# Kernel optimization log

Hardware: AMD Instinct MI355X
Metric: run time of the kernel (lower is better)

Reference implementation:

```python
import jax, jax.numpy as jnp
import numpy as np

N, D, A, K, E = 8192, 256, 1024, 65, 4096

def setup_inputs() -> dict:
    key = jax.random.key(0)
    ks = jax.random.split(key, 8)
    s = 0.02  # linear-init scale to keep activations sane
    return {
        "embedding": jax.random.normal(ks[0], (N, D), jnp.float32),
        "data": jax.random.randint(ks[1], (E, 2), 0, N, jnp.int64),
        "Wq": jax.random.normal(ks[2], (D, A), jnp.float32) * s,
        "bq": jnp.zeros((A,), jnp.float32),
        "Wk": jax.random.normal(ks[3], (D, A), jnp.float32) * s,
        "bk": jnp.zeros((A,), jnp.float32),
        "Wv": jax.random.normal(ks[4], (D, A), jnp.float32) * s,
        "bv": jnp.zeros((A,), jnp.float32),
        "W_edge": jax.random.normal(ks[5], (K, A, A), jnp.float32) * s,
    }

def reference(embedding, data, Wq, bq, Wk, bk, Wv, bv, W_edge):
    # NodeSelfAttention: dense full attention over all N nodes
    Q = embedding @ Wq + bq            # [N, A]
    Km = embedding @ Wk + bk           # [N, A]
    V = embedding @ Wv + bv            # [N, A]
    scale = 1.0 / jnp.sqrt(jnp.float32(D))  # note: sqrt(num_feats)=sqrt(256), as in source
    scores = (Q @ Km.T) * scale        # [N, N]
    attn = jax.nn.softmax(scores, axis=-1)
    attn_emb = attn @ V                # [N, A]
    # gather edge endpoints
    h_u = attn_emb[data[:, 0]]         # [E, A]
    h_v = attn_emb[data[:, 1]]         # [E, A]
    # KWayPred: out[e,k] = h_u[e] @ W_edge[k] @ h_v[e]
    # (source computes full ExE matmul per k and takes diag; this is the
    #  equivalent O(E*K*A^2) bilinear-diag form)
    t = jnp.einsum('ed,kdf->ekf', h_u, W_edge)   # [E, K, A]
    out = jnp.einsum('ekf,ef->ek', t, h_v)       # [E, K]
    return out
```

## Files before the change

### kernel.cpp

```cpp
#include <hip/hip_runtime.h>
#include <cstdio>
#include <cstdint>

#define NTOK 8192
#define DIM  256
#define AA   1024
#define KE   65
#define EE   4096

typedef unsigned short u16;
typedef __attribute__((ext_vector_type(4))) float   f32x4;
typedef __attribute__((ext_vector_type(8))) short   bf16x8;
typedef __attribute__((ext_vector_type(8))) unsigned short u16x8;

#define DEVI __device__ __forceinline__

DEVI u16 f2bf(float f) {
  union { float f; unsigned u; } x; x.f = f;
  unsigned r = x.u + 0x7FFFu + ((x.u >> 16) & 1u);
  return (u16)(r >> 16);
}
DEVI float bf2f(u16 h) {
  union { unsigned u; float f; } x; x.u = ((unsigned)h) << 16;
  return x.f;
}

DEVI void gload16(const void* g, void* l) {
  __builtin_amdgcn_global_load_lds(
      (const __attribute__((address_space(1))) void*)g,
      (__attribute__((address_space(3))) void*)l,
      16, 0, 0);
}

DEVI void barx() {
  asm volatile("" ::: "memory");
  __builtin_amdgcn_s_barrier();
  asm volatile("" ::: "memory");
}

DEVI void stage_half(const u16* __restrict__ g0, int ld, char* dst, int tid) {
#pragma unroll
  for (int rr = 0; rr < 2; ++rr) {
    int o = rr * 8192 + (tid >> 6) * 1024 + (tid & 63) * 16;
    int q = o ^ (((o >> 7) & 7) << 4);
    gload16(g0 + (size_t)(q >> 7) * ld + ((q & 127) >> 1),
            dst + rr * 8192 + (tid >> 6) * 1024);
  }
}

template<int EPI, int QMODE>
__global__ __launch_bounds__(512, 2)
void gemm8(const u16* __restrict__ A, int lda,
           const u16* __restrict__ B, int ldb,
           int MT, int NT, int K,
           u16* __restrict__ o_s, float scale, int ldc,
           const u16* __restrict__ Hu, float* __restrict__ o_e,
           int* __restrict__ qcnt)
{
  __shared__ __align__(16) char lds[131072];
  __shared__ int s_next[3];
  char* ldsA = lds;
  char* ldsB = lds + 65536;

  const int tid = threadIdx.x, lane = tid & 63, wave = tid >> 6;
  const int wm = (wave >> 2) * 128;
  const int wn = (wave & 3) * 64;
  const int wnl = (wave & 1) * 64;
  const int KT = K >> 6, KT2 = KT >> 1;
  const int r15 = lane & 15, g16 = (lane >> 4) << 4;

  int xcc;
  asm volatile("s_getreg_b32 %0, hwreg(20, 0, 32)" : "=s"(xcc));
  xcc &= 7;
  const int MPX = MT >> 3;
  const int NQ = NT >> 3, NR = NT & 7;

  const char* Ab_e = ldsA +         (wm >> 7) * 16384;
  const char* Ab_o = ldsA + 32768 + (wm >> 7) * 16384;
  const char* Bb_e = ldsB +         (wn >> 7) * 16384;
  const char* Bb_o = ldsB + 32768 + (wn >> 7) * 16384;

  int dxr = 0;
  auto pop_next = [&]() {
    while (dxr < 8) {
      const int qi = (xcc + dxr) & 7;
      int per, ntb = 0, ntc = 0;
      if constexpr (QMODE == 0) {
        per = (MT * NT) >> 3;
      } else {
        ntc = NQ + (qi < NR ? 1 : 0);
        ntb = qi * NQ + (qi < NR ? qi : NR);
        per = ntc * MT;
      }
      const int idx = atomicAdd(&qcnt[qi], 1);
      if (idx < per) {
        int mt, nt;
        if constexpr (QMODE == 0) {
          mt = qi * MPX + (idx % MPX); nt = idx / MPX;
        } else {
          const int srw = ntc << 3;
          const int sr = idx / srw, rem = idx - sr * srw;
          nt = ntb + (rem >> 3); mt = (sr << 3) + (rem & 7);
        }
        s_next[0] = mt * 256; s_next[1] = nt * 256; s_next[2] = 1;
        return;
      }
      ++dxr;
    }
    s_next[2] = 0;
  };

  if (tid == 0) pop_next();
  __syncthreads();
  int m0 = s_next[0], n0 = s_next[1];
  if (!s_next[2]) return;

#define STAGE_A2(tk, h) do { const int _tk = (tk); \
    if (_tk < KT) stage_half(A + (size_t)(m0 + (h)*128) * lda + (size_t)_tk*64, lda, \
                             ldsA + (_tk & 1) * 32768 + (h) * 16384, tid); \
    else if (have_n) stage_half(A + (size_t)(m0n + (h)*128) * lda + (size_t)(_tk-KT)*64, lda, \
                                ldsA + (_tk & 1) * 32768 + (h) * 16384, tid); } while (0)
#define STAGE_B2(tk, h) do { const int _tk = (tk); \
    if (_tk < KT) stage_half(B + (size_t)(n0 + (h)*128) * ldb + (size_t)_tk*64, ldb, \
                             ldsB + (_tk & 1) * 32768 + (h) * 16384, tid); \
    else if (have_n) stage_half(B + (size_t)(n0n + (h)*128) * ldb + (size_t)(_tk-KT)*64, ldb, \
                                ldsB + (_tk & 1) * 32768 + (h) * 16384, tid); } while (0)
#define RD_A4(base, q) \
  _Pragma("unroll") for (int m = (q)*4; m < (q)*4+4; ++m) \
  _Pragma("unroll") for (int kk = 0; kk < 2; ++kk) { \
    int p = (m*16 + r15)*128 + kk*64 + g16; p ^= ((p>>7)&7)<<4; \
    a[m][kk] = *(const bf16x8*)((base) + p); }
#define RD_B2(base, q) \
  _Pragma("unroll") for (int n = (q)*2; n < (q)*2+2; ++n) \
  _Pragma("unroll") for (int kk = 0; kk < 2; ++kk) { \
    int p = (wnl + n*16 + r15)*128 + kk*64 + g16; p ^= ((p>>7)&7)<<4; \
    b[n][kk] = *(const bf16x8*)((base) + p); }
#define MM(QM, QN) do { \
  __builtin_amdgcn_s_setprio(1); \
  _Pragma("unroll") for (int kk = 0; kk < 2; ++kk) \
  _Pragma("unroll") for (int m = 0; m < 4; ++m) \
  _Pragma("unroll") for (int n = 0; n < 2; ++n) \
    acc[(QM)*4+m][(QN)*2+n] = __builtin_amdgcn_mfma_f32_16x16x32_bf16( \
        a[(QM)*4+m][kk], b[(QN)*2+n][kk], acc[(QM)*4+m][(QN)*2+n], 0, 0, 0); \
  __builtin_amdgcn_s_setprio(0); } while (0)
#define WAIT_LGKM0 do { asm volatile("s_waitcnt lgkmcnt(0)" ::: "memory"); \
                        __builtin_amdgcn_sched_barrier(0); } while (0)
#define KTILE(t, AB, BB) do { \
     \
    RD_B2(BB, 0); RD_A4(AB, 0); \
    STAGE_B2((t) + 1, 1); \
    asm volatile("s_waitcnt lgkmcnt(8)" ::: "memory"); \
    barx(); WAIT_LGKM0; \
    MM(0, 0); \
    barx(); \
     \
    RD_B2(BB, 1); \
    barx(); WAIT_LGKM0; \
    MM(0, 1); \
    barx(); \
     \
    RD_A4(AB, 1); \
    STAGE_B2((t) + 2, 0); \
    barx(); WAIT_LGKM0; \
    MM(1, 1); \
    barx(); \
     \
    STAGE_A2((t) + 2, 0); \
    STAGE_A2((t) + 2, 1); \
    barx(); \
    __builtin_amdgcn_sched_barrier(0); \
    MM(1, 0); \
    if (vm6) asm volatile("s_waitcnt vmcnt(6)" ::: "memory"); \
    else     asm volatile("s_waitcnt vmcnt(0)" ::: "memory"); \
    barx(); } while (0)

  {
    const int m0n = 0, n0n = 0; const bool have_n = false; (void)m0n; (void)n0n; (void)have_n;
    STAGE_A2(0, 0); STAGE_A2(0, 1); STAGE_B2(0, 0); STAGE_B2(0, 1);
    STAGE_B2(1, 0); STAGE_A2(1, 0); STAGE_A2(1, 1);
  }
  asm volatile("s_waitcnt vmcnt(6)" ::: "memory");
  barx();

  while (true) {
    f32x4 acc[8][4];
#pragma unroll
    for (int m = 0; m < 8; ++m)
#pragma unroll
      for (int n = 0; n < 4; ++n) acc[m][n] = f32x4{0.f, 0.f, 0.f, 0.f};

    int m0n = 0, n0n = 0;
    bool have_n = false;

    for (int i = 0; i < KT2; ++i) {
      const int ta = 2 * i, tb = 2 * i + 1;
      if (i == KT2 - 2 && tid == 0) pop_next();
      if (i == KT2 - 1) { m0n = s_next[0]; n0n = s_next[1]; have_n = (s_next[2] != 0); }
      const bool tail = (i == KT2 - 1);
      const bool vm6 = !tail || have_n;
      bf16x8 a[8][2], b[4][2];
      KTILE(ta, Ab_e, Bb_e);
      KTILE(tb, Ab_o, Bb_o);
    }

    const int rgrp = lane >> 4, cid = lane & 15;
    if constexpr (EPI == 1) {
#pragma unroll
      for (int m = 0; m < 8; ++m)
#pragma unroll
        for (int n = 0; n < 4; ++n)
#pragma unroll
          for (int j = 0; j < 4; ++j) {
            int row = m0 + wm + m * 16 + rgrp * 4 + j;
            int col = n0 + wn + n * 16 + cid;
            o_s[(size_t)row * ldc + col] = f2bf(acc[m][n][j] * scale);
          }
    } else {
      const int kidx  = n0 >> 10;
      const int dbase = (n0 & 1023) + wn;
#pragma unroll
      for (int m = 0; m < 8; ++m)
#pragma unroll
        for (int j = 0; j < 4; ++j) {
          int row = m0 + wm + m * 16 + rgrp * 4 + j;
          float p = 0.f;
#pragma unroll
          for (int n = 0; n < 4; ++n)
            p += acc[m][n][j] * bf2f(Hu[(size_t)row * AA + dbase + n * 16 + cid]);
          p += __shfl_xor(p, 1, 64);
          p += __shfl_xor(p, 2, 64);
          p += __shfl_xor(p, 4, 64);
          p += __shfl_xor(p, 8, 64);
          if (cid == 0) atomicAdd(&o_e[(size_t)row * KE + kidx], p);
        }
    }

    if (!have_n) break;
    m0 = m0n; n0 = n0n;
  }
#undef STAGE_A2
#undef STAGE_B2
#undef RD_A4
#undef RD_B2
#undef MM
#undef WAIT_LGKM0
#undef KTILE
}

#define BM 128
#define BN 128
#define BK 64

template<int EPI, bool BF32>
__global__ __launch_bounds__(256)
void gemm_bt(const u16* __restrict__ A, int lda,
             const void* __restrict__ Bptr, int ldb,
             int MT, int NT, int K,
             u16* __restrict__ o_q, u16* __restrict__ o_k, u16* __restrict__ o_vt,
             const float* __restrict__ biasc,
             u16* __restrict__ o_s, float scale, int ldc,
             const u16* __restrict__ Hu, float* __restrict__ o_e)
{
  const int nb  = MT * NT;
  const int per = nb >> 3;
  int bid = blockIdx.x;
  bid = (bid & 7) * per + (bid >> 3);
  const int mt = bid % MT, nt = bid / MT;
  const int m0 = mt * BM, n0 = nt * BN;

  __shared__ u16 As[BM * BK];
  __shared__ u16 Bs[BN * BK];

  const int tid  = threadIdx.x;
  const int lane = tid & 63, wave = tid >> 6;
  const int wm = (wave >> 1) * 64, wn = (wave & 1) * 64;

  f32x4 acc[4][4];
#pragma unroll
  for (int m = 0; m < 4; ++m)
#pragma unroll
    for (int n = 0; n < 4; ++n) acc[m][n] = f32x4{0.f, 0.f, 0.f, 0.f};

  const u16*   Bh = (const u16*)Bptr;
  const float* Bf = (const float*)Bptr;

  const int KT = K / BK;
  for (int kt = 0; kt < KT; ++kt) {
    const int k0 = kt * BK;
#pragma unroll
    for (int it = 0; it < 4; ++it) {
      int o = it * 4096 + wave * 1024 + lane * 16;
      int r = o >> 7;
      int c = (o & 127) >> 1;
      gload16(A + (size_t)(m0 + r) * lda + k0 + c,
              &As[(it * 4096 + wave * 1024) >> 1]);
    }
    if constexpr (!BF32) {
#pragma unroll
      for (int it = 0; it < 4; ++it) {
        int o = it * 4096 + wave * 1024 + lane * 16;
        int r = o >> 7;
        int c = (o & 127) >> 1;
        gload16(Bh + (size_t)(n0 + r) * ldb + k0 + c,
                &Bs[(it * 4096 + wave * 1024) >> 1]);
      }
    } else {
#pragma unroll
      for (int it = 0; it < 8; ++it) {
        int e = it * 1024 + tid * 4;
        int r = e >> 6, c = e & 63;
        const float4 v = *(const float4*)(Bf + (size_t)(n0 + r) * ldb + k0 + c);
        ushort4 h;
        h.x = f2bf(v.x); h.y = f2bf(v.y); h.z = f2bf(v.z); h.w = f2bf(v.w);
        *(ushort4*)&Bs[r * BK + c] = h;
      }
    }
    asm volatile("s_waitcnt vmcnt(0)" ::: "memory");
    __syncthreads();

#pragma unroll
    for (int kk = 0; kk < 2; ++kk) {
      const int ro = lane & 15;
      const int ko = kk * 32 + (lane >> 4) * 8;
      bf16x8 af[4], bfg[4];
#pragma unroll
      for (int m = 0; m < 4; ++m)
        af[m] = *(const bf16x8*)&As[(wm + m * 16 + ro) * BK + ko];
#pragma unroll
      for (int n = 0; n < 4; ++n)
        bfg[n] = *(const bf16x8*)&Bs[(wn + n * 16 + ro) * BK + ko];
#pragma unroll
      for (int m = 0; m < 4; ++m)
#pragma unroll
        for (int n = 0; n < 4; ++n)
          acc[m][n] = __builtin_amdgcn_mfma_f32_16x16x32_bf16(
              af[m], bfg[n], acc[m][n], 0, 0, 0);
    }
    __syncthreads();
  }

  const int rgrp = lane >> 4, cid = lane & 15;

  if constexpr (EPI == 0) {
#pragma unroll
    for (int m = 0; m < 4; ++m)
#pragma unroll
      for (int n = 0; n < 4; ++n)
#pragma unroll
        for (int j = 0; j < 4; ++j) {
          int row = m0 + wm + m * 16 + rgrp * 4 + j;
          int col = n0 + wn + n * 16 + cid;
          float v = acc[m][n][j] + biasc[col];
          u16 h = f2bf(v);
          if (col < 1024)       o_q[(size_t)row * AA + col] = h;
          else if (col < 2048)  o_k[(size_t)row * AA + (col - 1024)] = h;
          else                  o_vt[(size_t)(col - 2048) * NTOK + row] = h;
        }
  } else if constexpr (EPI == 1) {
#pragma unroll
    for (int m = 0; m < 4; ++m)
#pragma unroll
      for (int n = 0; n < 4; ++n)
#pragma unroll
        for (int j = 0; j < 4; ++j) {
          int row = m0 + wm + m * 16 + rgrp * 4 + j;
          int col = n0 + wn + n * 16 + cid;
          o_s[(size_t)row * ldc + col] = f2bf(acc[m][n][j] * scale);
        }
  } else {
    const int kidx  = n0 >> 10;
    const int dbase = (n0 & 1023) + wn;
#pragma unroll
    for (int m = 0; m < 4; ++m)
#pragma unroll
      for (int j = 0; j < 4; ++j) {
        int row = m0 + wm + m * 16 + rgrp * 4 + j;
        float p = 0.f;
#pragma unroll
        for (int n = 0; n < 4; ++n) {
          int d = dbase + n * 16 + cid;
          p += acc[m][n][j] * bf2f(Hu[(size_t)row * AA + d]);
        }
        p += __shfl_xor(p, 1, 64);
        p += __shfl_xor(p, 2, 64);
        p += __shfl_xor(p, 4, 64);
        p += __shfl_xor(p, 8, 64);
        if (cid == 0) atomicAdd(&o_e[(size_t)row * KE + kidx], p);
      }
  }
}

__global__ __launch_bounds__(256)
void softmax_rows(u16* __restrict__ S)
{
  const size_t base = (size_t)blockIdx.x * 8192;
  const int tid = threadIdx.x;
  const int lane = tid & 63, wave = tid >> 6;
  float v[32];
#pragma unroll
  for (int c = 0; c < 4; ++c) {
    u16x8 u = *(const u16x8*)&S[base + c * 2048 + tid * 8];
#pragma unroll
    for (int j = 0; j < 8; ++j) v[c * 8 + j] = bf2f(u[j]);
  }
  float mx = -1e30f;
#pragma unroll
  for (int i = 0; i < 32; ++i) mx = fmaxf(mx, v[i]);
#pragma unroll
  for (int off = 1; off < 64; off <<= 1) mx = fmaxf(mx, __shfl_xor(mx, off, 64));
  __shared__ float r1[4], r2[4];
  if (lane == 0) r1[wave] = mx;
  __syncthreads();
  mx = fmaxf(fmaxf(r1[0], r1[1]), fmaxf(r1[2], r1[3]));

  float s = 0.f;
#pragma unroll
  for (int i = 0; i < 32; ++i) { v[i] = __expf(v[i] - mx); s += v[i]; }
#pragma unroll
  for (int off = 1; off < 64; off <<= 1) s += __shfl_xor(s, off, 64);
  if (lane == 0) r2[wave] = s;
  __syncthreads();
  s = r2[0] + r2[1] + r2[2] + r2[3];
  const float inv = 1.f / s;
#pragma unroll
  for (int c = 0; c < 4; ++c) {
    u16x8 u;
#pragma unroll
    for (int j = 0; j < 8; ++j) u[j] = f2bf(v[c * 8 + j] * inv);
    *(u16x8*)&S[base + c * 2048 + tid * 8] = u;
  }
}

__global__ __launch_bounds__(256)
void gather_rows(const unsigned* __restrict__ dw, const u16* __restrict__ AE,
                 u16* __restrict__ Hu, u16* __restrict__ Hv)
{
  bool i64 = true;
#pragma unroll
  for (int w = 1; w < 32; w += 2) i64 = i64 && (dw[w] == 0u);
  const int e = blockIdx.x;
  const unsigned iu = i64 ? dw[4 * e]     : dw[2 * e];
  const unsigned iv = i64 ? dw[4 * e + 2] : dw[2 * e + 1];
  const int t = threadIdx.x;
  *(ushort4*)&Hu[(size_t)e * AA + t * 4] = *(const ushort4*)&AE[(size_t)iu * AA + t * 4];
  *(ushort4*)&Hv[(size_t)e * AA + t * 4] = *(const ushort4*)&AE[(size_t)iv * AA + t * 4];
}

__global__ __launch_bounds__(256)
void init_misc(float* __restrict__ out_e, const float* __restrict__ bq,
               const float* __restrict__ bk, const float* __restrict__ bv,
               float* __restrict__ biasc, int* __restrict__ qall)
{
  const int i = blockIdx.x * 256 + threadIdx.x;
  if (i < EE * KE) out_e[i] = 0.f;
  if (i < 1024) {
    biasc[i]        = bq[i];
    biasc[1024 + i] = bk[i];
    biasc[2048 + i] = bv[i];
  }
  if (i < 64) qall[i] = 0;
}

__global__ __launch_bounds__(256)
void cvt_f32_bf16_v4(const float* __restrict__ src, u16* __restrict__ dst, int n4)
{
  for (int i = blockIdx.x * 256 + threadIdx.x; i < n4; i += gridDim.x * 256) {
    float4 v = ((const float4*)src)[i];
    ushort4 h; h.x = f2bf(v.x); h.y = f2bf(v.y); h.z = f2bf(v.z); h.w = f2bf(v.w);
    ((ushort4*)dst)[i] = h;
  }
}

__global__ __launch_bounds__(256)
void build_wT(const float* __restrict__ Wq, const float* __restrict__ Wk,
              const float* __restrict__ Wv, u16* __restrict__ WT)
{
  const int nn = blockIdx.x;
  const int d  = threadIdx.x;
  const float* W = (nn < 1024) ? Wq : ((nn < 2048) ? Wk : Wv);
  WT[nn * DIM + d] = f2bf(W[(size_t)d * AA + (nn & 1023)]);
}

extern "C" void kernel_launch(void* const* d_in, const int* in_sizes, int n_in,
                              void* d_out, int out_size, void* d_ws, size_t ws_size,
                              hipStream_t stream)
{
  (void)in_sizes; (void)out_size;
  if (n_in < 9) return;
  const float*    emb  = (const float*)d_in[0];
  const unsigned* data = (const unsigned*)d_in[1];
  const float* Wq = (const float*)d_in[2];
  const float* bq = (const float*)d_in[3];
  const float* Wk = (const float*)d_in[4];
  const float* bk = (const float*)d_in[5];
  const float* Wv = (const float*)d_in[6];
  const float* bv = (const float*)d_in[7];
  const float* We = (const float*)d_in[8];
  float* out = (float*)d_out;

  char* ws = (char*)d_ws;
  size_t off = 0;
  auto alloc = [&](size_t bytes) -> void* {
    void* p = ws + off;
    off += (bytes + 255) & ~(size_t)255;
    return p;
  };
  u16*   emb_b = (u16*)alloc((size_t)NTOK * DIM * 2);
  u16*   WT    = (u16*)alloc((size_t)3072 * DIM * 2);
  float* biasc = (float*)alloc(3072 * 4);
  int*   qall  = (int*)alloc(64 * 4);
  u16*   Qb    = (u16*)alloc((size_t)NTOK * AA * 2);
  u16*   Kb    = (u16*)alloc((size_t)NTOK * AA * 2);
  u16*   Vt    = (u16*)alloc((size_t)AA * NTOK * 2);
  u16*   AE    = (u16*)alloc((size_t)NTOK * AA * 2);
  u16*   Hu    = (u16*)alloc((size_t)EE * AA * 2);
  u16*   Hv    = (u16*)alloc((size_t)EE * AA * 2);

  const size_t webf_bytes = ((size_t)KE * AA * AA * 2 + 255) & ~(size_t)255;
  u16* We_b = nullptr;
  if (off + webf_bytes + (size_t)1024 * NTOK * 2 <= ws_size) {
    We_b = (u16*)(ws + off);
    off += webf_bytes;
  }

  int chunk = 4096;
  while (chunk > 128 && off + (size_t)chunk * NTOK * 2 > ws_size) chunk >>= 1;
  u16* Sc = (u16*)alloc((size_t)chunk * NTOK * 2);
  if (off > ws_size) {
    fprintf(stderr, "kernel_launch: ws too small (need %zu, have %zu)\n", off, ws_size);
    return;
  }

  init_misc<<<(EE * KE) / 256, 256, 0, stream>>>(out, bq, bk, bv, biasc, qall);
  cvt_f32_bf16_v4<<<2048, 256, 0, stream>>>(emb, emb_b, NTOK * DIM / 4);
  build_wT<<<3072, 256, 0, stream>>>(Wq, Wk, Wv, WT);
  if (We_b)
    cvt_f32_bf16_v4<<<4096, 256, 0, stream>>>(We, We_b, KE * AA * AA / 4);

  gemm_bt<0, false><<<64 * 24, 256, 0, stream>>>(
      emb_b, DIM, WT, DIM, 64, 24, DIM,
      Qb, Kb, Vt, biasc, nullptr, 0.f, 0, nullptr, nullptr);

  const int nch = NTOK / chunk;
  for (int ci = 0; ci < nch; ++ci) {
    const u16* Qc = Qb + (size_t)ci * chunk * AA;
    const bool big = ((chunk & 2047) == 0);
    if (big)
      gemm8<1, 1><<<256, 512, 0, stream>>>(
          Qc, AA, Kb, AA, chunk / 256, 32, AA,
          Sc, 0.0625f, NTOK, nullptr, nullptr, qall + 8 * ci);
    else
      gemm_bt<1, false><<<(chunk / 128) * 64, 256, 0, stream>>>(
          Qc, AA, Kb, AA, chunk / 128, 64, AA,
          nullptr, nullptr, nullptr, nullptr, Sc, 0.0625f, NTOK, nullptr, nullptr);
    softmax_rows<<<chunk, 256, 0, stream>>>(Sc);
    gemm_bt<1, false><<<(chunk / 128) * 8, 256, 0, stream>>>(
        Sc, NTOK, Vt, NTOK, chunk / 128, 8, NTOK,
        nullptr, nullptr, nullptr, nullptr,
        AE + (size_t)ci * chunk * AA, 1.0f, AA, nullptr, nullptr);
  }

  gather_rows<<<EE, 256, 0, stream>>>(data, AE, Hu, Hv);

  if (We_b)
    gemm8<2, 1><<<256, 512, 0, stream>>>(
        Hv, AA, We_b, AA, 16, 260, AA,
        nullptr, 0.f, 0, Hu, out, qall + 32);
  else
    gemm_bt<3, true><<<32 * 520, 256, 0, stream>>>(
        Hv, AA, We, AA, 32, 520, AA,
        nullptr, nullptr, nullptr, nullptr, nullptr, 0.f, 0, Hu, out);
}
```

Baseline: 1.486 ms.

## Use 128x128-tile persistent GEMM kernel for edge bilinear stage

Adds a new persistent, XCC-aware GEMM kernel (gemm4) with 256 threads, 128x128 tiles and double-buffered 64-wide K staging. It replaces the 256x256-tile 512-thread gemm8 for the final edge-weight bilinear GEMM with fused Hu dot-product epilogue. Smaller tiles double the tile count and may improve load balance and occupancy. In exchange, each tile reuses less data and issues more atomics in the epilogue.

```diff
diff --git a/kernel.cpp b/kernel.cpp
--- a/kernel.cpp
+++ b/kernel.cpp
@@ -45,6 +45,159 @@
     int q = o ^ (((o >> 7) & 7) << 4);
     gload16(g0 + (size_t)(q >> 7) * ld + ((q & 127) >> 1),
             dst + rr * 8192 + (tid >> 6) * 1024);
+  }
+}
+
+DEVI void stage_t4(const u16* __restrict__ g0, int ld, char* dst, int tid) {
+#pragma unroll
+  for (int rr = 0; rr < 4; ++rr) {
+    int o = rr * 4096 + tid * 16;
+    int q = o ^ (((o >> 7) & 7) << 4);
+    gload16(g0 + (size_t)(q >> 7) * ld + ((q & 127) >> 1),
+            dst + rr * 4096 + (tid >> 6) * 1024);
+  }
+}
+
+template<int EPI, int QMODE>
+__global__ __launch_bounds__(256, 2)
+void gemm4(const u16* __restrict__ A, int lda,
+           const u16* __restrict__ B, int ldb,
+           int MT, int NT, int K,
+           u16* __restrict__ o_s, float scale, int ldc,
+           const u16* __restrict__ Hu, float* __restrict__ o_e,
+           int* __restrict__ qcnt)
+{
+  __shared__ __align__(16) char lds[65536];
+  __shared__ int s_idx;
+  char* ldsA = lds;
+  char* ldsB = lds + 32768;
+
+  const int tid = threadIdx.x, lane = tid & 63, wave = tid >> 6;
+  const int wm = (wave >> 1) * 64, wn = (wave & 1) * 64;
+  const int KT = K >> 6;
+  const int r15 = lane & 15, g16 = (lane >> 4) << 4;
+
+  int xcc;
+  asm volatile("s_getreg_b32 %0, hwreg(20, 0, 32)" : "=s"(xcc));
+  xcc &= 7;
+  const int MPX = MT >> 3;
+  const int NQ = NT >> 3, NR = NT & 7;
+
+  for (int dx = 0; dx < 8; ++dx) {
+    const int qi = (xcc + dx) & 7;
+    int per, ntb = 0, ntc = 0;
+    if constexpr (QMODE == 0) {
+      per = (MT * NT) >> 3;
+    } else {
+      ntc = NQ + (qi < NR ? 1 : 0);
+      ntb = qi * NQ + (qi < NR ? qi : NR);
+      per = ntc * MT;
+    }
+    while (true) {
+      if (tid == 0) s_idx = atomicAdd(&qcnt[qi], 1);
+      __syncthreads();
+      const int idx = s_idx;
+      __syncthreads();
+      if (idx >= per) break;
+      int mt, nt;
+      if constexpr (QMODE == 0) {
+        mt = qi * MPX + (idx % MPX); nt = idx / MPX;
+      } else {
+        const int srw = ntc << 3;
+        const int sr = idx / srw, rem = idx - sr * srw;
+        nt = ntb + (rem >> 3); mt = (sr << 3) + (rem & 7);
+      }
+      const int m0 = mt * 128, n0 = nt * 128;
+      const u16* Ag = A + (size_t)m0 * lda;
+      const u16* Bg = B + (size_t)n0 * ldb;
+
+      f32x4 acc[4][4];
+#pragma unroll
+      for (int m = 0; m < 4; ++m)
+#pragma unroll
+        for (int n = 0; n < 4; ++n) acc[m][n] = f32x4{0.f, 0.f, 0.f, 0.f};
+
+      stage_t4(Ag,      lda, ldsA,         tid);
+      stage_t4(Bg,      ldb, ldsB,         tid);
+      stage_t4(Ag + 64, lda, ldsA + 16384, tid);
+      stage_t4(Bg + 64, ldb, ldsB + 16384, tid);
+      asm volatile("s_waitcnt vmcnt(8)" ::: "memory");
+      barx();
+
+      for (int t = 0; t < KT; ++t) {
+        const char* Ab = ldsA + (t & 1) * 16384;
+        const char* Bb = ldsB + (t & 1) * 16384;
+        bf16x8 a[4][2], b[4][2];
+#pragma unroll
+        for (int m = 0; m < 4; ++m)
+#pragma unroll
+          for (int kk = 0; kk < 2; ++kk) {
+            int p = (wm + m * 16 + r15) * 128 + kk * 64 + g16;
+            p ^= ((p >> 7) & 7) << 4;
+            a[m][kk] = *(const bf16x8*)(Ab + p);
+          }
+#pragma unroll
+        for (int n = 0; n < 4; ++n)
+#pragma unroll
+          for (int kk = 0; kk < 2; ++kk) {
+            int p = (wn + n * 16 + r15) * 128 + kk * 64 + g16;
+            p ^= ((p >> 7) & 7) << 4;
+            b[n][kk] = *(const bf16x8*)(Bb + p);
+          }
+        asm volatile("s_waitcnt lgkmcnt(0)" ::: "memory");
+        __builtin_amdgcn_sched_barrier(0);
+        barx();
+        if (t + 2 < KT) {
+          stage_t4(Ag + (size_t)(t + 2) * 64, lda, ldsA + (t & 1) * 16384, tid);
+          stage_t4(Bg + (size_t)(t + 2) * 64, ldb, ldsB + (t & 1) * 16384, tid);
+        }
+        __builtin_amdgcn_s_setprio(1);
+#pragma unroll
+        for (int kk = 0; kk < 2; ++kk)
+#pragma unroll
+          for (int m = 0; m < 4; ++m)
+#pragma unroll
+            for (int n = 0; n < 4; ++n)
+              acc[m][n] = __builtin_amdgcn_mfma_f32_16x16x32_bf16(
+                  a[m][kk], b[n][kk], acc[m][n], 0, 0, 0);
+        __builtin_amdgcn_s_setprio(0);
+        if (t + 2 < KT) asm volatile("s_waitcnt vmcnt(8)" ::: "memory");
+        else            asm volatile("s_waitcnt vmcnt(0)" ::: "memory");
+        barx();
+      }
+
+      const int rgrp = lane >> 4, cid = lane & 15;
+      if constexpr (EPI == 1) {
+#pragma unroll
+        for (int m = 0; m < 4; ++m)
+#pragma unroll
+          for (int n = 0; n < 4; ++n)
+#pragma unroll
+            for (int j = 0; j < 4; ++j) {
+              int row = m0 + wm + m * 16 + rgrp * 4 + j;
+              int col = n0 + wn + n * 16 + cid;
+              o_s[(size_t)row * ldc + col] = f2bf(acc[m][n][j] * scale);
+            }
+      } else {
+        const int kidx  = n0 >> 10;
+        const int dbase = (n0 & 1023) + wn;
+#pragma unroll
+        for (int m = 0; m < 4; ++m)
+#pragma unroll
+          for (int j = 0; j < 4; ++j) {
+            int row = m0 + wm + m * 16 + rgrp * 4 + j;
+            float p = 0.f;
+#pragma unroll
+            for (int n = 0; n < 4; ++n)
+              p += acc[m][n][j] * bf2f(Hu[(size_t)row * AA + dbase + n * 16 + cid]);
+            p += __shfl_xor(p, 1, 64);
+            p += __shfl_xor(p, 2, 64);
+            p += __shfl_xor(p, 4, 64);
+            p += __shfl_xor(p, 8, 64);
+            if (cid == 0) atomicAdd(&o_e[(size_t)row * KE + kidx], p);
+          }
+      }
+    }
   }
 }
 
@@ -146,25 +299,21 @@
 #define WAIT_LGKM0 do { asm volatile("s_waitcnt lgkmcnt(0)" ::: "memory"); \
                         __builtin_amdgcn_sched_barrier(0); } while (0)
 #define KTILE(t, AB, BB) do { \
-     \
     RD_B2(BB, 0); RD_A4(AB, 0); \
     STAGE_B2((t) + 1, 1); \
     asm volatile("s_waitcnt lgkmcnt(8)" ::: "memory"); \
     barx(); WAIT_LGKM0; \
     MM(0, 0); \
     barx(); \
-     \
     RD_B2(BB, 1); \
     barx(); WAIT_LGKM0; \
     MM(0, 1); \
     barx(); \
-     \
     RD_A4(AB, 1); \
     STAGE_B2((t) + 2, 0); \
     barx(); WAIT_LGKM0; \
     MM(1, 1); \
     barx(); \
-     \
     STAGE_A2((t) + 2, 0); \
     STAGE_A2((t) + 2, 1); \
     barx(); \
@@ -563,8 +712,8 @@
   gather_rows<<<EE, 256, 0, stream>>>(data, AE, Hu, Hv);
 
   if (We_b)
-    gemm8<2, 1><<<256, 512, 0, stream>>>(
-        Hv, AA, We_b, AA, 16, 260, AA,
+    gemm4<2, 1><<<512, 256, 0, stream>>>(
+        Hv, AA, We_b, AA, 32, 520, AA,
         nullptr, 0.f, 0, Hu, out, qall + 32);
   else
     gemm_bt<3, true><<<32 * 520, 256, 0, stream>>>(
```

After: 1.518 ms. 2.2% more time.

## Replace persistent atomic work-queue GEMM with one-tile-per-block launch

Applied to the files above, without the earlier changes.

Removes the persistent gemm8 kernel, which used per-XCD atomic queues to pop 256x256 tiles and prefetch the next tile's K-slices across tile boundaries. It is replaced with gemm8s, which launches one block per tile and maps block IDs to tiles with an XCD-aware swizzle. This drops the queue counters, their zeroing and the atomics. In exchange it gives up the cross-tile prefetch overlap and pays per-block launch, prologue and epilogue costs for many more blocks.

```diff
diff --git a/kernel.cpp b/kernel.cpp
--- a/kernel.cpp
+++ b/kernel.cpp
@@ -48,83 +48,42 @@
   }
 }
 
-template<int EPI, int QMODE>
+template<int EPI>
 __global__ __launch_bounds__(512, 2)
-void gemm8(const u16* __restrict__ A, int lda,
-           const u16* __restrict__ B, int ldb,
-           int MT, int NT, int K,
-           u16* __restrict__ o_s, float scale, int ldc,
-           const u16* __restrict__ Hu, float* __restrict__ o_e,
-           int* __restrict__ qcnt)
+void gemm8s(const u16* __restrict__ A, int lda,
+            const u16* __restrict__ B, int ldb,
+            int MT, int NT, int K,
+            u16* __restrict__ o_s, float scale, int ldc,
+            const u16* __restrict__ Hu, float* __restrict__ o_e)
 {
   __shared__ __align__(16) char lds[131072];
-  __shared__ int s_next[3];
   char* ldsA = lds;
   char* ldsB = lds + 65536;
+
+  const int nb = MT * NT, per = nb >> 3;
+  int bid = blockIdx.x;
+  bid = (bid & 7) * per + (bid >> 3);
+  const int mt = bid % MT, nt = bid / MT;
+  const int m0 = mt * 256, n0 = nt * 256;
 
   const int tid = threadIdx.x, lane = tid & 63, wave = tid >> 6;
   const int wm = (wave >> 2) * 128;
   const int wn = (wave & 3) * 64;
   const int wnl = (wave & 1) * 64;
-  const int KT = K >> 6, KT2 = KT >> 1;
+  const int KT = K >> 6;
   const int r15 = lane & 15, g16 = (lane >> 4) << 4;
-
-  int xcc;
-  asm volatile("s_getreg_b32 %0, hwreg(20, 0, 32)" : "=s"(xcc));
-  xcc &= 7;
-  const int MPX = MT >> 3;
-  const int NQ = NT >> 3, NR = NT & 7;
 
   const char* Ab_e = ldsA +         (wm >> 7) * 16384;
   const char* Ab_o = ldsA + 32768 + (wm >> 7) * 16384;
   const char* Bb_e = ldsB +         (wn >> 7) * 16384;
   const char* Bb_o = ldsB + 32768 + (wn >> 7) * 16384;
 
-  int dxr = 0;
-  auto pop_next = [&]() {
-    while (dxr < 8) {
-      const int qi = (xcc + dxr) & 7;
-      int per, ntb = 0, ntc = 0;
-      if constexpr (QMODE == 0) {
-        per = (MT * NT) >> 3;
-      } else {
-        ntc = NQ + (qi < NR ? 1 : 0);
-        ntb = qi * NQ + (qi < NR ? qi : NR);
-        per = ntc * MT;
-      }
-      const int idx = atomicAdd(&qcnt[qi], 1);
-      if (idx < per) {
-        int mt, nt;
-        if constexpr (QMODE == 0) {
-          mt = qi * MPX + (idx % MPX); nt = idx / MPX;
-        } else {
-          const int srw = ntc << 3;
-          const int sr = idx / srw, rem = idx - sr * srw;
-          nt = ntb + (rem >> 3); mt = (sr << 3) + (rem & 7);
-        }
-        s_next[0] = mt * 256; s_next[1] = nt * 256; s_next[2] = 1;
-        return;
-      }
-      ++dxr;
-    }
-    s_next[2] = 0;
-  };
-
-  if (tid == 0) pop_next();
-  __syncthreads();
-  int m0 = s_next[0], n0 = s_next[1];
-  if (!s_next[2]) return;
-
 #define STAGE_A2(tk, h) do { const int _tk = (tk); \
     if (_tk < KT) stage_half(A + (size_t)(m0 + (h)*128) * lda + (size_t)_tk*64, lda, \
-                             ldsA + (_tk & 1) * 32768 + (h) * 16384, tid); \
-    else if (have_n) stage_half(A + (size_t)(m0n + (h)*128) * lda + (size_t)(_tk-KT)*64, lda, \
-                                ldsA + (_tk & 1) * 32768 + (h) * 16384, tid); } while (0)
+                             ldsA + (_tk & 1) * 32768 + (h) * 16384, tid); } while (0)
 #define STAGE_B2(tk, h) do { const int _tk = (tk); \
     if (_tk < KT) stage_half(B + (size_t)(n0 + (h)*128) * ldb + (size_t)_tk*64, ldb, \
-                             ldsB + (_tk & 1) * 32768 + (h) * 16384, tid); \
-    else if (have_n) stage_half(B + (size_t)(n0n + (h)*128) * ldb + (size_t)(_tk-KT)*64, ldb, \
-                                ldsB + (_tk & 1) * 32768 + (h) * 16384, tid); } while (0)
+                             ldsB + (_tk & 1) * 32768 + (h) * 16384, tid); } while (0)
 #define RD_A4(base, q) \
   _Pragma("unroll") for (int m = (q)*4; m < (q)*4+4; ++m) \
   _Pragma("unroll") for (int kk = 0; kk < 2; ++kk) { \
@@ -170,73 +129,58 @@
     barx(); \
     __builtin_amdgcn_sched_barrier(0); \
     MM(1, 0); \
-    if (vm6) asm volatile("s_waitcnt vmcnt(6)" ::: "memory"); \
-    else     asm volatile("s_waitcnt vmcnt(0)" ::: "memory"); \
+    if ((t) + 2 < KT) asm volatile("s_waitcnt vmcnt(6)" ::: "memory"); \
+    else              asm volatile("s_waitcnt vmcnt(0)" ::: "memory"); \
     barx(); } while (0)
 
-  {
-    const int m0n = 0, n0n = 0; const bool have_n = false; (void)m0n; (void)n0n; (void)have_n;
-    STAGE_A2(0, 0); STAGE_A2(0, 1); STAGE_B2(0, 0); STAGE_B2(0, 1);
-    STAGE_B2(1, 0); STAGE_A2(1, 0); STAGE_A2(1, 1);
-  }
+  f32x4 acc[8][4];
+#pragma unroll
+  for (int m = 0; m < 8; ++m)
+#pragma unroll
+    for (int n = 0; n < 4; ++n) acc[m][n] = f32x4{0.f, 0.f, 0.f, 0.f};
+
+  STAGE_A2(0, 0); STAGE_A2(0, 1); STAGE_B2(0, 0); STAGE_B2(0, 1);
+  STAGE_B2(1, 0); STAGE_A2(1, 0); STAGE_A2(1, 1);
   asm volatile("s_waitcnt vmcnt(6)" ::: "memory");
   barx();
 
-  while (true) {
-    f32x4 acc[8][4];
+  for (int i = 0; i < (KT >> 1); ++i) {
+    const int ta = 2 * i, tb = 2 * i + 1;
+    bf16x8 a[8][2], b[4][2];
+    KTILE(ta, Ab_e, Bb_e);
+    KTILE(tb, Ab_o, Bb_o);
+  }
+
+  const int rgrp = lane >> 4, cid = lane & 15;
+  if constexpr (EPI == 1) {
 #pragma unroll
     for (int m = 0; m < 8; ++m)
 #pragma unroll
-      for (int n = 0; n < 4; ++n) acc[m][n] = f32x4{0.f, 0.f, 0.f, 0.f};
-
-    int m0n = 0, n0n = 0;
-    bool have_n = false;
-
-    for (int i = 0; i < KT2; ++i) {
-      const int ta = 2 * i, tb = 2 * i + 1;
-      if (i == KT2 - 2 && tid == 0) pop_next();
-      if (i == KT2 - 1) { m0n = s_next[0]; n0n = s_next[1]; have_n = (s_next[2] != 0); }
-      const bool tail = (i == KT2 - 1);
-      const bool vm6 = !tail || have_n;
-      bf16x8 a[8][2], b[4][2];
-      KTILE(ta, Ab_e, Bb_e);
-      KTILE(tb, Ab_o, Bb_o);
-    }
-
-    const int rgrp = lane >> 4, cid = lane & 15;
-    if constexpr (EPI == 1) {
-#pragma unroll
-      for (int m = 0; m < 8; ++m)
-#pragma unroll
-        for (int n = 0; n < 4; ++n)
-#pragma unroll
-          for (int j = 0; j < 4; ++j) {
-            int row = m0 + wm + m * 16 + rgrp * 4 + j;
-            int col = n0 + wn + n * 16 + cid;
-            o_s[(size_t)row * ldc + col] = f2bf(acc[m][n][j] * scale);
-          }
-    } else {
-      const int kidx  = n0 >> 10;
-      const int dbase = (n0 & 1023) + wn;
-#pragma unroll
-      for (int m = 0; m < 8; ++m)
+      for (int n = 0; n < 4; ++n)
 #pragma unroll
         for (int j = 0; j < 4; ++j) {
           int row = m0 + wm + m * 16 + rgrp * 4 + j;
-          float p = 0.f;
-#pragma unroll
-          for (int n = 0; n < 4; ++n)
-            p += acc[m][n][j] * bf2f(Hu[(size_t)row * AA + dbase + n * 16 + cid]);
-          p += __shfl_xor(p, 1, 64);
-          p += __shfl_xor(p, 2, 64);
-          p += __shfl_xor(p, 4, 64);
-          p += __shfl_xor(p, 8, 64);
-          if (cid == 0) atomicAdd(&o_e[(size_t)row * KE + kidx], p);
+          int col = n0 + wn + n * 16 + cid;
+          o_s[(size_t)row * ldc + col] = f2bf(acc[m][n][j] * scale);
         }
-    }
-
-    if (!have_n) break;
-    m0 = m0n; n0 = n0n;
+  } else {
+    const int kidx  = n0 >> 10;
+    const int dbase = (n0 & 1023) + wn;
+#pragma unroll
+    for (int m = 0; m < 8; ++m)
+#pragma unroll
+      for (int j = 0; j < 4; ++j) {
+        int row = m0 + wm + m * 16 + rgrp * 4 + j;
+        float p = 0.f;
+#pragma unroll
+        for (int n = 0; n < 4; ++n)
+          p += acc[m][n][j] * bf2f(Hu[(size_t)row * AA + dbase + n * 16 + cid]);
+        p += __shfl_xor(p, 1, 64);
+        p += __shfl_xor(p, 2, 64);
+        p += __shfl_xor(p, 4, 64);
+        p += __shfl_xor(p, 8, 64);
+        if (cid == 0) atomicAdd(&o_e[(size_t)row * KE + kidx], p);
+      }
   }
 #undef STAGE_A2
 #undef STAGE_B2
@@ -449,7 +393,7 @@
 __global__ __launch_bounds__(256)
 void init_misc(float* __restrict__ out_e, const float* __restrict__ bq,
                const float* __restrict__ bk, const float* __restrict__ bv,
-               float* __restrict__ biasc, int* __restrict__ qall)
+               float* __restrict__ biasc)
 {
   const int i = blockIdx.x * 256 + threadIdx.x;
   if (i < EE * KE) out_e[i] = 0.f;
@@ -458,7 +402,6 @@
     biasc[1024 + i] = bk[i];
     biasc[2048 + i] = bv[i];
   }
-  if (i < 64) qall[i] = 0;
 }
 
 __global__ __launch_bounds__(256)
@@ -508,7 +451,6 @@
   u16*   emb_b = (u16*)alloc((size_t)NTOK * DIM * 2);
   u16*   WT    = (u16*)alloc((size_t)3072 * DIM * 2);
   float* biasc = (float*)alloc(3072 * 4);
-  int*   qall  = (int*)alloc(64 * 4);
   u16*   Qb    = (u16*)alloc((size_t)NTOK * AA * 2);
   u16*   Kb    = (u16*)alloc((size_t)NTOK * AA * 2);
   u16*   Vt    = (u16*)alloc((size_t)AA * NTOK * 2);
@@ -531,7 +473,7 @@
     return;
   }
 
-  init_misc<<<(EE * KE) / 256, 256, 0, stream>>>(out, bq, bk, bv, biasc, qall);
+  init_misc<<<(EE * KE) / 256, 256, 0, stream>>>(out, bq, bk, bv, biasc);
   cvt_f32_bf16_v4<<<2048, 256, 0, stream>>>(emb, emb_b, NTOK * DIM / 4);
   build_wT<<<3072, 256, 0, stream>>>(Wq, Wk, Wv, WT);
   if (We_b)
@@ -546,9 +488,9 @@
     const u16* Qc = Qb + (size_t)ci * chunk * AA;
     const bool big = ((chunk & 2047) == 0);
     if (big)
-      gemm8<1, 1><<<256, 512, 0, stream>>>(
+      gemm8s<1><<<(chunk / 256) * 32, 512, 0, stream>>>(
           Qc, AA, Kb, AA, chunk / 256, 32, AA,
-          Sc, 0.0625f, NTOK, nullptr, nullptr, qall + 8 * ci);
+          Sc, 0.0625f, NTOK, nullptr, nullptr);
     else
       gemm_bt<1, false><<<(chunk / 128) * 64, 256, 0, stream>>>(
           Qc, AA, Kb, AA, chunk / 128, 64, AA,
@@ -563,9 +505,9 @@
   gather_rows<<<EE, 256, 0, stream>>>(data, AE, Hu, Hv);
 
   if (We_b)
-    gemm8<2, 1><<<256, 512, 0, stream>>>(
+    gemm8s<2><<<16 * 260, 512, 0, stream>>>(
         Hv, AA, We_b, AA, 16, 260, AA,
-        nullptr, 0.f, 0, Hu, out, qall + 32);
+        nullptr, 0.f, 0, Hu, out);
   else
     gemm_bt<3, true><<<32 * 520, 256, 0, stream>>>(
         Hv, AA, We, AA, 32, 520, AA,
```

Measured after the change: 1.421 ms. -4.4%, faster.
